# Kernel tuning notes

Hardware: AMD Instinct MI355X
Metric: run time of the kernel (lower is better)

## Reference

```python
import jax, jax.numpy as jnp
import numpy as np

N_QUBITS = 12
N_LAYERS = 4
SCALE = 1.0
BATCH = 256


def setup_inputs() -> dict:
    key = jax.random.key(0)
    k1, k2, k3 = jax.random.split(key, 3)
    return {
        "x": jax.random.normal(k1, (BATCH, N_QUBITS), dtype=jnp.float32),
        "weights": jax.random.normal(k2, (N_LAYERS, N_QUBITS, 3), dtype=jnp.float32),
        "entanglers": jax.random.uniform(k3, (N_LAYERS, N_QUBITS), dtype=jnp.float32),
    }


def _ry(theta):
    # theta: () or (B,) -> (..., 2, 2) complex64.  RY = [[c,-s],[s,c]]
    c = jnp.cos(theta / 2)
    s = jnp.sin(theta / 2)
    return jnp.stack([jnp.stack([c, -s], -1), jnp.stack([s, c], -1)], -2).astype(jnp.complex64)


def _rz(theta):
    # RZ = diag(e^{-i t/2}, e^{+i t/2})
    e = jnp.exp(-1j * theta.astype(jnp.complex64) / 2)
    z = jnp.zeros_like(e)
    return jnp.stack([jnp.stack([e, z], -1), jnp.stack([z, jnp.conj(e)], -1)], -2)


def _apply_1q(psi, U, q, n):
    # psi: (B, 2**n), wire 0 = most significant bit (PennyLane convention)
    B = psi.shape[0]
    psi = psi.reshape(B, 2 ** q, 2, 2 ** (n - q - 1))
    if U.ndim == 2:  # shared gate (weights)
        psi = jnp.einsum("ij,bajc->baic", U, psi)
    else:  # per-sample gate (inputs)
        psi = jnp.einsum("bij,bajc->baic", U, psi)
    return psi.reshape(B, 2 ** n)


def _apply_cnot(psi, c, t, n):
    # control c, target t (distinct), handles wrap-around since moveaxis is general
    B = psi.shape[0]
    psi = psi.reshape((B,) + (2,) * n)
    psi = jnp.moveaxis(psi, (c + 1, t + 1), (1, 2))
    shp = psi.shape
    psi = psi.reshape(B, 2, 2, -1)
    psi = jnp.stack([psi[:, 0], psi[:, 1, ::-1]], axis=1)  # flip target where control=1
    psi = psi.reshape(shp)
    psi = jnp.moveaxis(psi, (1, 2), (c + 1, t + 1))
    return psi.reshape(B, 2 ** n)


def reference(x, weights, entanglers):
    n = N_QUBITS
    B = x.shape[0]
    pi = jnp.float32(np.pi)
    psi = jnp.zeros((B, 2 ** n), jnp.complex64).at[:, 0].set(1.0)
    # encoding: RY(x_i * pi) then RZ(x_i^2 * pi) per qubit (per-sample gates)
    for q in range(n):
        psi = _apply_1q(psi, _ry(x[:, q] * pi), q, n)
        psi = _apply_1q(psi, _rz((x[:, q] ** 2) * pi), q, n)
    mask = entanglers > 0.5
    for layer in range(N_LAYERS):
        for q in range(n):
            phi, th, om = weights[layer, q, 0], weights[layer, q, 1], weights[layer, q, 2]
            U = _rz(om) @ _ry(th) @ _rz(phi)  # PennyLane Rot(phi, theta, omega)
            psi = _apply_1q(psi, U, q, n)
        for q in range(n):
            psi2 = _apply_cnot(psi, q, (q + 1) % n, n)
            psi = jnp.where(mask[layer, q], psi2, psi)
    probs = psi.real ** 2 + psi.imag ** 2  # (B, 2**n)
    # <Z_q> = sum_s p(s) * (1 - 2*bit_q(s)); wire 0 is MSB
    bits = (jnp.arange(2 ** n)[:, None] >> jnp.arange(n - 1, -1, -1)[None, :]) & 1
    signs = (1 - 2 * bits).astype(jnp.float32)  # (2**n, n)
    return (probs @ signs) * jnp.float32(SCALE)
```

## Files before the change

kernel.cpp:

```cpp
#include <hip/hip_runtime.h>
#include <math.h>

constexpr int NQ  = 12;
constexpr int NS  = 1 << NQ;
constexpr int NL  = 4;
constexpr int BLK = 256;
constexpr int R   = 16;
constexpr float PI_F = 3.14159265358979323846f;


typedef float c32 __attribute__((ext_vector_type(2)));

__device__ __forceinline__ c32 cmul(c32 a, c32 b) {
    c32 t = (c32){-a.y, a.y} * b.yx;
    return (c32){a.x, a.x} * b + t;
}
struct cg { c32 xx, ny; };
__device__ __forceinline__ cg mkg(c32 u) {
    cg g; g.xx = (c32){u.x, u.x}; g.ny = (c32){-u.y, u.y}; return g;
}
__device__ __forceinline__ c32 cmulg(cg g, c32 b) { return g.xx * b + g.ny * b.yx; }
__device__ __forceinline__ c32 cmadg(cg g, c32 b, c32 c) { return g.xx * b + (g.ny * b.yx + c); }

__device__ __forceinline__ void sfence() { __builtin_amdgcn_sched_barrier(0); }

template<int CTRL>
__device__ __forceinline__ float dppmov(float v) {
    return __int_as_float(__builtin_amdgcn_mov_dpp(__float_as_int(v), CTRL, 0xF, 0xF, false));
}
__device__ __forceinline__ float dppx4(float v) {
    int s = __float_as_int(v);
    int o = __builtin_amdgcn_update_dpp(s, s, 0x104, 0xF, 0x5, false);
    o     = __builtin_amdgcn_update_dpp(o, s, 0x114, 0xF, 0xA, false);
    return __int_as_float(o);
}

#if __has_builtin(__builtin_amdgcn_permlane16_swap)
#define HAVE_PL16 1
#endif
#if __has_builtin(__builtin_amdgcn_permlane32_swap)
#define HAVE_PL32 1
#endif

template<int M>
__device__ __forceinline__ float lanex(float v, int tid) {
    if constexpr (M == 1)  return dppmov<0xB1>(v);
    else if constexpr (M == 2)  return dppmov<0x4E>(v);
    else if constexpr (M == 4)  return dppx4(v);
    else if constexpr (M == 8)  return dppmov<0x128>(v);
    else if constexpr (M == 16) {
#ifdef HAVE_PL16
        auto r = __builtin_amdgcn_permlane16_swap(__float_as_int(v), __float_as_int(v), false, false);
        return __int_as_float((tid & 16) ? r[0] : r[1]);
#else
        return __shfl_xor(v, 16, 64);
#endif
    } else {
#ifdef HAVE_PL32
        auto r = __builtin_amdgcn_permlane32_swap(__float_as_int(v), __float_as_int(v), false, false);
        return __int_as_float((tid & 32) ? r[0] : r[1]);
#else
        return __shfl_xor(v, 32, 64);
#endif
    }
}
template<int M>
__device__ __forceinline__ c32 cx(c32 v, int tid) {
    return (c32){lanex<M>(v.x, tid), lanex<M>(v.y, tid)};
}

template<int P>
__device__ __forceinline__ void gate_reg(c32* v, const c32* u) {
    const cg g00 = mkg(u[0]), g01 = mkg(u[1]), g10 = mkg(u[2]), g11 = mkg(u[3]);
    #pragma unroll
    for (int r = 0; r < R; ++r)
        if (!(r & (1 << P))) {
            c32 a = v[r], b = v[r | (1 << P)];
            v[r]            = cmadg(g01, b, cmulg(g00, a));
            v[r | (1 << P)] = cmadg(g11, b, cmulg(g10, a));
        }
}

template<int M>
__device__ __forceinline__ void gate_lane(c32* v, int tid, const c32* u) {
    const bool hi = tid & M;
    const c32 Ud = hi ? u[3] : u[0];
    const c32 Uo = hi ? u[2] : u[1];
    const cg gd = mkg(Ud), go = mkg(Uo);
    c32 o[R];
    #pragma unroll
    for (int r = 0; r < R; ++r) o[r] = cx<M>(v[r], tid);
    sfence();
    #pragma unroll
    for (int r = 0; r < R; ++r) v[r] = cmadg(gd, v[r], cmulg(go, o[r]));
}

template<int CM, int TM>
__device__ __forceinline__ void cnot_ll(c32* v, int tid) {
    if (tid & CM) {
        c32 o[R];
        #pragma unroll
        for (int r = 0; r < R; ++r) o[r] = cx<TM>(v[r], tid);
        sfence();
        #pragma unroll
        for (int r = 0; r < R; ++r) v[r] = o[r];
    }
}

template<int PC, int PT>
__device__ __forceinline__ void cnot_rr(c32* v) {
    #pragma unroll
    for (int r = 0; r < R; ++r)
        if ((r & (1 << PC)) && !(r & (1 << PT))) {
            c32 t = v[r]; v[r] = v[r ^ (1 << PT)]; v[r ^ (1 << PT)] = t;
        }
}

__global__ __launch_bounds__(BLK, 1)
void qsim_kernel(const float* __restrict__ x,
                 const float* __restrict__ w,
                 const float* __restrict__ ent,
                 float* __restrict__ out)
{
    __shared__ c32  xbuf[NS];
    __shared__ c32  gmat[NL * NQ][4];
    __shared__ c32  uenc[NQ][2];
    __shared__ int  entf[NL * NQ];
    __shared__ float redbuf[4 * NQ];

    const int tid = threadIdx.x;
    const int b   = blockIdx.x;

    if (tid < NL * NQ) {
        float phi = w[tid * 3 + 0], th = w[tid * 3 + 1], om = w[tid * 3 + 2];
        float s, c;   sincosf(0.5f * th, &s, &c);
        float sa, ca; sincosf(0.5f * (phi + om), &sa, &ca);
        float sm, cm; sincosf(0.5f * (phi - om), &sm, &cm);
        gmat[tid][0] = (c32){ c * ca, -c * sa};
        gmat[tid][1] = (c32){-s * cm, -s * sm};
        gmat[tid][2] = (c32){ s * cm, -s * sm};
        gmat[tid][3] = (c32){ c * ca,  c * sa};
        entf[tid] = ent[tid] > 0.5f;
    }
    if (tid >= 64 && tid < 64 + NQ) {
        int q = tid - 64;
        float xv = x[b * NQ + q];
        float s, c;   sincosf(0.5f * PI_F * xv, &s, &c);
        float zs, zc; sincosf(0.5f * PI_F * xv * xv, &zs, &zc);
        uenc[q][0] = (c32){c * zc, -c * zs};
        uenc[q][1] = (c32){s * zc,  s * zs};
    }
    __syncthreads();

    c32 A = uenc[0][(tid >> 7) & 1];
    #pragma unroll
    for (int q = 1; q < 8; ++q) A = cmul(A, uenc[q][(tid >> (7 - q)) & 1]);
    c32 AP[4], PAB[4];
    #pragma unroll
    for (int j = 0; j < 4; ++j)
        AP[j] = cmul(A, cmul(uenc[8][j >> 1], uenc[9][j & 1]));
    #pragma unroll
    for (int k = 0; k < 4; ++k)
        PAB[k] = cmul(uenc[10][k >> 1], uenc[11][k & 1]);
    c32 v[R];
    #pragma unroll
    for (int r = 0; r < R; ++r) v[r] = cmul(AP[(r >> 2) & 3], PAB[r & 3]);

    const int lane_slot = tid & 63;
    const int g         = tid >> 6;

    #pragma unroll 1
    for (int layer = 0; layer < NL; ++layer) {
        const int gb = layer * NQ;

        {
            #pragma unroll
            for (int r = 0; r < R; ++r) xbuf[r * BLK + tid] = v[r];

            const c32* Ua = gmat[gb + 0];
            const c32* Ub = gmat[gb + 1];
            const int  gp = (entf[gb + 0] && (g & 2)) ? (g ^ 1) : g;
            const int  ar = (gp >> 1) * 2, br = (gp & 1) * 2;
            c32 K0 = cmul(Ua[ar + ( g      >> 1)], Ub[br + ( g      & 1)]);
            c32 K1 = cmul(Ua[ar + ((g ^ 1) >> 1)], Ub[br + ((g ^ 1) & 1)]);
            c32 K2 = cmul(Ua[ar + ((g ^ 2) >> 1)], Ub[br + ((g ^ 2) & 1)]);
            c32 K3 = cmul(Ua[ar + ((g ^ 3) >> 1)], Ub[br + ((g ^ 3) & 1)]);
            const bool pf = (layer > 0) && entf[gb - 1];
            const cg gE0 = mkg(K0), gE1 = mkg(K1), gE2 = mkg(K2), gE3 = mkg(K3);
            const cg gO0 = mkg(pf ? K2 : K0), gO1 = mkg(pf ? K3 : K1);
            const cg gO2 = mkg(pf ? K0 : K2), gO3 = mkg(pf ? K1 : K3);

            const c32* p1 = xbuf + ((g ^ 1) << 6) + lane_slot;
            const c32* p2 = xbuf + ((g ^ 2) << 6) + lane_slot;
            const c32* p3 = xbuf + ((g ^ 3) << 6) + lane_slot;

            __syncthreads();
            c32 b1[R], b2[R], b3[R];
            #pragma unroll
            for (int r = 0; r < R; ++r) b1[r] = p1[r * BLK];
            #pragma unroll
            for (int r = 0; r < R; ++r) b2[r] = p2[r * BLK];
            #pragma unroll
            for (int r = 0; r < R; ++r) b3[r] = p3[r * BLK];
            sfence();
            #pragma unroll
            for (int r = 0; r < R; ++r) {
                c32 acc;
                if (r & 1) {
                    acc = cmulg(gO0, v[r]);
                    acc = cmadg(gO1, b1[r], acc);
                    acc = cmadg(gO2, b2[r], acc);
                    acc = cmadg(gO3, b3[r], acc);
                } else {
                    acc = cmulg(gE0, v[r]);
                    acc = cmadg(gE1, b1[r], acc);
                    acc = cmadg(gE2, b2[r], acc);
                    acc = cmadg(gE3, b3[r], acc);
                }
                v[r] = acc;
            }
            __syncthreads();
        }

        gate_lane<32>(v, tid, gmat[gb + 2]);
        gate_lane<16>(v, tid, gmat[gb + 3]);
        gate_lane< 8>(v, tid, gmat[gb + 4]);
        gate_lane< 4>(v, tid, gmat[gb + 5]);
        gate_lane< 2>(v, tid, gmat[gb + 6]);
        gate_lane< 1>(v, tid, gmat[gb + 7]);
        gate_reg<3>(v, gmat[gb + 8]);
        gate_reg<2>(v, gmat[gb + 9]);
        gate_reg<1>(v, gmat[gb + 10]);
        gate_reg<0>(v, gmat[gb + 11]);

        if (entf[gb + 1] && (tid & 64)) {
            c32 o[R];
            #pragma unroll
            for (int r = 0; r < R; ++r) o[r] = cx<32>(v[r], tid);
            sfence();
            #pragma unroll
            for (int r = 0; r < R; ++r) v[r] = o[r];
        }
        if (entf[gb + 2]) cnot_ll<32, 16>(v, tid);
        if (entf[gb + 3]) cnot_ll<16,  8>(v, tid);
        if (entf[gb + 4]) cnot_ll< 8,  4>(v, tid);
        if (entf[gb + 5]) cnot_ll< 4,  2>(v, tid);
        if (entf[gb + 6]) cnot_ll< 2,  1>(v, tid);
        if (entf[gb + 7]) {
            const bool c_ = tid & 1;
            #pragma unroll
            for (int r = 0; r < 8; ++r) {
                c32 a = v[r], bb = v[r | 8];
                v[r]     = c_ ? bb : a;
                v[r | 8] = c_ ? a  : bb;
            }
        }
        if (entf[gb + 8])  cnot_rr<3, 2>(v);
        if (entf[gb + 9])  cnot_rr<2, 1>(v);
        if (entf[gb + 10]) cnot_rr<1, 0>(v);
    }

    const bool e011L = entf[(NL - 1) * NQ + 11];
    const int  t7    = (tid >> 7) & 1;

    float pr[R];
    #pragma unroll
    for (int r = 0; r < R; ++r) {
        c32 p = v[r] * v[r];
        pr[r] = p.x + p.y;
    }
    float S = 0.f, acc0 = 0.f;
    #pragma unroll
    for (int r = 0; r < R; ++r) {
        S += pr[r];
        const int s11 = t7 ^ (e011L & (r & 1));
        acc0 += s11 ? -pr[r] : pr[r];
    }
    float T[4];
    #pragma unroll
    for (int pb = 0; pb < 4; ++pb) {
        float t = 0.f;
        #pragma unroll
        for (int r = 0; r < R; ++r) t += ((r >> pb) & 1) ? -pr[r] : pr[r];
        T[pb] = t;
    }

    float contrib[NQ];
    contrib[0] = acc0;
    #pragma unroll
    for (int q = 1; q < 8; ++q) contrib[q] = ((tid >> (7 - q)) & 1) ? -S : S;
    contrib[8] = T[3]; contrib[9] = T[2]; contrib[10] = T[1]; contrib[11] = T[0];

    #pragma unroll
    for (int step = 0; step < 6; ++step) {
        float o[NQ];
        #pragma unroll
        for (int q = 0; q < NQ; ++q) {
            switch (step) {
                case 0: o[q] = lanex< 1>(contrib[q], tid); break;
                case 1: o[q] = lanex< 2>(contrib[q], tid); break;
                case 2: o[q] = lanex< 4>(contrib[q], tid); break;
                case 3: o[q] = lanex< 8>(contrib[q], tid); break;
                case 4: o[q] = lanex<16>(contrib[q], tid); break;
                default: o[q] = lanex<32>(contrib[q], tid); break;
            }
        }
        #pragma unroll
        for (int q = 0; q < NQ; ++q) contrib[q] += o[q];
    }
    if ((tid & 63) == 0) {
        const int wv = tid >> 6;
        #pragma unroll
        for (int q = 0; q < NQ; ++q) redbuf[wv * NQ + q] = contrib[q];
    }
    __syncthreads();
    if (tid < NQ)
        out[b * NQ + tid] = redbuf[tid] + redbuf[NQ + tid] + redbuf[2 * NQ + tid] + redbuf[3 * NQ + tid];
}

extern "C" void kernel_launch(void* const* d_in, const int* in_sizes, int n_in,
                              void* d_out, int out_size, void* d_ws, size_t ws_size,
                              hipStream_t stream) {
    const float* x   = (const float*)d_in[0];
    const float* w   = (const float*)d_in[1];
    const float* ent = (const float*)d_in[2];
    float* out = (float*)d_out;
    const int B = in_sizes[0] / NQ;
    qsim_kernel<<<B, BLK, 0, stream>>>(x, w, ent, out);
}
```

Before: 78.44 us.

## Double threads per block, halve registers per thread, fuse three qubits in LDS stage

Raises the block to 512 threads with 8 amplitudes per thread instead of 16, so qubits 0-2 are spread across wave groups. The LDS exchange stage now applies a fused three-qubit gate (an 8x8 Kronecker product with the CNOT permutations folded in) through shared memory, replacing the earlier two-qubit version. The aim is more waves per CU and fewer registers per thread to hide latency. The cost is 8-term complex accumulations per amplitude and more LDS reads per element, and the reduction now spans 8 waves.

```diff
diff --git a/kernel.cpp b/kernel.cpp
--- a/kernel.cpp
+++ b/kernel.cpp
@@ -4,8 +4,8 @@
 constexpr int NQ  = 12;
 constexpr int NS  = 1 << NQ;
 constexpr int NL  = 4;
-constexpr int BLK = 256;
-constexpr int R   = 16;
+constexpr int BLK = 512;
+constexpr int R   = 8;
 constexpr float PI_F = 3.14159265358979323846f;
 
 
@@ -116,7 +116,7 @@
         }
 }
 
-__global__ __launch_bounds__(BLK, 1)
+__global__ __launch_bounds__(BLK, 2)
 void qsim_kernel(const float* __restrict__ x,
                  const float* __restrict__ w,
                  const float* __restrict__ ent,
@@ -126,7 +126,7 @@
     __shared__ c32  gmat[NL * NQ][4];
     __shared__ c32  uenc[NQ][2];
     __shared__ int  entf[NL * NQ];
-    __shared__ float redbuf[4 * NQ];
+    __shared__ float redbuf[8 * NQ];
 
     const int tid = threadIdx.x;
     const int b   = blockIdx.x;
@@ -152,19 +152,16 @@
     }
     __syncthreads();
 
-    c32 A = uenc[0][(tid >> 7) & 1];
-    #pragma unroll
-    for (int q = 1; q < 8; ++q) A = cmul(A, uenc[q][(tid >> (7 - q)) & 1]);
-    c32 AP[4], PAB[4];
-    #pragma unroll
-    for (int j = 0; j < 4; ++j)
-        AP[j] = cmul(A, cmul(uenc[8][j >> 1], uenc[9][j & 1]));
-    #pragma unroll
-    for (int k = 0; k < 4; ++k)
-        PAB[k] = cmul(uenc[10][k >> 1], uenc[11][k & 1]);
+    c32 A = uenc[0][(tid >> 8) & 1];
+    #pragma unroll
+    for (int q = 1; q < 9; ++q) A = cmul(A, uenc[q][(tid >> (8 - q)) & 1]);
+    c32 PB[R];
+    #pragma unroll
+    for (int k = 0; k < R; ++k)
+        PB[k] = cmul(uenc[9][(k >> 2) & 1], cmul(uenc[10][(k >> 1) & 1], uenc[11][k & 1]));
     c32 v[R];
     #pragma unroll
-    for (int r = 0; r < R; ++r) v[r] = cmul(AP[(r >> 2) & 3], PAB[r & 3]);
+    for (int r = 0; r < R; ++r) v[r] = cmul(A, PB[r]);
 
     const int lane_slot = tid & 63;
     const int g         = tid >> 6;
@@ -179,61 +176,126 @@
 
             const c32* Ua = gmat[gb + 0];
             const c32* Ub = gmat[gb + 1];
-            const int  gp = (entf[gb + 0] && (g & 2)) ? (g ^ 1) : g;
-            const int  ar = (gp >> 1) * 2, br = (gp & 1) * 2;
-            c32 K0 = cmul(Ua[ar + ( g      >> 1)], Ub[br + ( g      & 1)]);
-            c32 K1 = cmul(Ua[ar + ((g ^ 1) >> 1)], Ub[br + ((g ^ 1) & 1)]);
-            c32 K2 = cmul(Ua[ar + ((g ^ 2) >> 1)], Ub[br + ((g ^ 2) & 1)]);
-            c32 K3 = cmul(Ua[ar + ((g ^ 3) >> 1)], Ub[br + ((g ^ 3) & 1)]);
+            const c32* Uc = gmat[gb + 2];
+            int gp = (entf[gb + 1] && (g & 2)) ? (g ^ 1) : g;
+            gp     = (entf[gb + 0] && (gp & 4)) ? (gp ^ 2) : gp;
+            const int ar = (gp >> 2) * 2;
+            const int br = ((gp >> 1) & 1) * 2;
+            const int cr = (gp & 1) * 2;
+            cg gE[8];
+            #pragma unroll
+            for (int m = 0; m < 8; ++m) {
+                const int j = g ^ m;
+                c32 kk = cmul(Ua[ar + (j >> 2)],
+                          cmul(Ub[br + ((j >> 1) & 1)], Uc[cr + (j & 1)]));
+                gE[m] = mkg(kk);
+            }
             const bool pf = (layer > 0) && entf[gb - 1];
-            const cg gE0 = mkg(K0), gE1 = mkg(K1), gE2 = mkg(K2), gE3 = mkg(K3);
-            const cg gO0 = mkg(pf ? K2 : K0), gO1 = mkg(pf ? K3 : K1);
-            const cg gO2 = mkg(pf ? K0 : K2), gO3 = mkg(pf ? K1 : K3);
-
-            const c32* p1 = xbuf + ((g ^ 1) << 6) + lane_slot;
-            const c32* p2 = xbuf + ((g ^ 2) << 6) + lane_slot;
-            const c32* p3 = xbuf + ((g ^ 3) << 6) + lane_slot;
+
+            const c32* px = xbuf + lane_slot;
 
             __syncthreads();
-            c32 b1[R], b2[R], b3[R];
-            #pragma unroll
-            for (int r = 0; r < R; ++r) b1[r] = p1[r * BLK];
-            #pragma unroll
-            for (int r = 0; r < R; ++r) b2[r] = p2[r * BLK];
-            #pragma unroll
-            for (int r = 0; r < R; ++r) b3[r] = p3[r * BLK];
-            sfence();
-            #pragma unroll
-            for (int r = 0; r < R; ++r) {
-                c32 acc;
-                if (r & 1) {
-                    acc = cmulg(gO0, v[r]);
-                    acc = cmadg(gO1, b1[r], acc);
-                    acc = cmadg(gO2, b2[r], acc);
-                    acc = cmadg(gO3, b3[r], acc);
-                } else {
-                    acc = cmulg(gE0, v[r]);
-                    acc = cmadg(gE1, b1[r], acc);
-                    acc = cmadg(gE2, b2[r], acc);
-                    acc = cmadg(gE3, b3[r], acc);
+            {
+                c32 bm[7][4];
+                #pragma unroll
+                for (int m = 1; m < 8; ++m) {
+                    const c32* pp = px + ((g ^ m) << 6);
+                    #pragma unroll
+                    for (int r = 0; r < 4; ++r) bm[m - 1][r] = pp[r * BLK];
                 }
-                v[r] = acc;
+                sfence();
+                #pragma unroll
+                for (int r = 0; r < 4; ++r) {
+                    c32 acc;
+                    if (!(r & 1)) {
+                        acc = cmulg(gE[0], v[r]);
+                        acc = cmadg(gE[1], bm[0][r], acc);
+                        acc = cmadg(gE[2], bm[1][r], acc);
+                        acc = cmadg(gE[3], bm[2][r], acc);
+                        acc = cmadg(gE[4], bm[3][r], acc);
+                        acc = cmadg(gE[5], bm[4][r], acc);
+                        acc = cmadg(gE[6], bm[5][r], acc);
+                        acc = cmadg(gE[7], bm[6][r], acc);
+                    } else if (!pf) {
+                        acc = cmulg(gE[0], v[r]);
+                        acc = cmadg(gE[1], bm[0][r], acc);
+                        acc = cmadg(gE[2], bm[1][r], acc);
+                        acc = cmadg(gE[3], bm[2][r], acc);
+                        acc = cmadg(gE[4], bm[3][r], acc);
+                        acc = cmadg(gE[5], bm[4][r], acc);
+                        acc = cmadg(gE[6], bm[5][r], acc);
+                        acc = cmadg(gE[7], bm[6][r], acc);
+                    } else {
+                        acc = cmulg(gE[4], v[r]);
+                        acc = cmadg(gE[5], bm[0][r], acc);
+                        acc = cmadg(gE[6], bm[1][r], acc);
+                        acc = cmadg(gE[7], bm[2][r], acc);
+                        acc = cmadg(gE[0], bm[3][r], acc);
+                        acc = cmadg(gE[1], bm[4][r], acc);
+                        acc = cmadg(gE[2], bm[5][r], acc);
+                        acc = cmadg(gE[3], bm[6][r], acc);
+                    }
+                    v[r] = acc;
+                }
+            }
+            {
+                c32 bm[7][4];
+                #pragma unroll
+                for (int m = 1; m < 8; ++m) {
+                    const c32* pp = px + ((g ^ m) << 6) + 4 * BLK;
+                    #pragma unroll
+                    for (int r = 0; r < 4; ++r) bm[m - 1][r] = pp[r * BLK];
+                }
+                sfence();
+                #pragma unroll
+                for (int rr = 0; rr < 4; ++rr) {
+                    const int r = rr + 4;
+                    c32 acc;
+                    if (!(r & 1)) {
+                        acc = cmulg(gE[0], v[r]);
+                        acc = cmadg(gE[1], bm[0][rr], acc);
+                        acc = cmadg(gE[2], bm[1][rr], acc);
+                        acc = cmadg(gE[3], bm[2][rr], acc);
+                        acc = cmadg(gE[4], bm[3][rr], acc);
+                        acc = cmadg(gE[5], bm[4][rr], acc);
+                        acc = cmadg(gE[6], bm[5][rr], acc);
+                        acc = cmadg(gE[7], bm[6][rr], acc);
+                    } else if (!pf) {
+                        acc = cmulg(gE[0], v[r]);
+                        acc = cmadg(gE[1], bm[0][rr], acc);
+                        acc = cmadg(gE[2], bm[1][rr], acc);
+                        acc = cmadg(gE[3], bm[2][rr], acc);
+                        acc = cmadg(gE[4], bm[3][rr], acc);
+                        acc = cmadg(gE[5], bm[4][rr], acc);
+                        acc = cmadg(gE[6], bm[5][rr], acc);
+                        acc = cmadg(gE[7], bm[6][rr], acc);
+                    } else {
+                        acc = cmulg(gE[4], v[r]);
+                        acc = cmadg(gE[5], bm[0][rr], acc);
+                        acc = cmadg(gE[6], bm[1][rr], acc);
+                        acc = cmadg(gE[7], bm[2][rr], acc);
+                        acc = cmadg(gE[0], bm[3][rr], acc);
+                        acc = cmadg(gE[1], bm[4][rr], acc);
+                        acc = cmadg(gE[2], bm[5][rr], acc);
+                        acc = cmadg(gE[3], bm[6][rr], acc);
+                    }
+                    v[r] = acc;
+                }
             }
             __syncthreads();
         }
 
-        gate_lane<32>(v, tid, gmat[gb + 2]);
-        gate_lane<16>(v, tid, gmat[gb + 3]);
-        gate_lane< 8>(v, tid, gmat[gb + 4]);
-        gate_lane< 4>(v, tid, gmat[gb + 5]);
-        gate_lane< 2>(v, tid, gmat[gb + 6]);
-        gate_lane< 1>(v, tid, gmat[gb + 7]);
-        gate_reg<3>(v, gmat[gb + 8]);
+        gate_lane<32>(v, tid, gmat[gb + 3]);
+        gate_lane<16>(v, tid, gmat[gb + 4]);
+        gate_lane< 8>(v, tid, gmat[gb + 5]);
+        gate_lane< 4>(v, tid, gmat[gb + 6]);
+        gate_lane< 2>(v, tid, gmat[gb + 7]);
+        gate_lane< 1>(v, tid, gmat[gb + 8]);
         gate_reg<2>(v, gmat[gb + 9]);
         gate_reg<1>(v, gmat[gb + 10]);
         gate_reg<0>(v, gmat[gb + 11]);
 
-        if (entf[gb + 1] && (tid & 64)) {
+        if (entf[gb + 2] && (tid & 64)) {
             c32 o[R];
             #pragma unroll
             for (int r = 0; r < R; ++r) o[r] = cx<32>(v[r], tid);
@@ -241,27 +303,26 @@
             #pragma unroll
             for (int r = 0; r < R; ++r) v[r] = o[r];
         }
-        if (entf[gb + 2]) cnot_ll<32, 16>(v, tid);
-        if (entf[gb + 3]) cnot_ll<16,  8>(v, tid);
-        if (entf[gb + 4]) cnot_ll< 8,  4>(v, tid);
-        if (entf[gb + 5]) cnot_ll< 4,  2>(v, tid);
-        if (entf[gb + 6]) cnot_ll< 2,  1>(v, tid);
-        if (entf[gb + 7]) {
+        if (entf[gb + 3]) cnot_ll<32, 16>(v, tid);
+        if (entf[gb + 4]) cnot_ll<16,  8>(v, tid);
+        if (entf[gb + 5]) cnot_ll< 8,  4>(v, tid);
+        if (entf[gb + 6]) cnot_ll< 4,  2>(v, tid);
+        if (entf[gb + 7]) cnot_ll< 2,  1>(v, tid);
+        if (entf[gb + 8]) {
             const bool c_ = tid & 1;
             #pragma unroll
-            for (int r = 0; r < 8; ++r) {
-                c32 a = v[r], bb = v[r | 8];
+            for (int r = 0; r < 4; ++r) {
+                c32 a = v[r], bb = v[r | 4];
                 v[r]     = c_ ? bb : a;
-                v[r | 8] = c_ ? a  : bb;
-            }
-        }
-        if (entf[gb + 8])  cnot_rr<3, 2>(v);
+                v[r | 4] = c_ ? a  : bb;
+            }
+        }
         if (entf[gb + 9])  cnot_rr<2, 1>(v);
         if (entf[gb + 10]) cnot_rr<1, 0>(v);
     }
 
     const bool e011L = entf[(NL - 1) * NQ + 11];
-    const int  t7    = (tid >> 7) & 1;
+    const int  t8    = (tid >> 8) & 1;
 
     float pr[R];
     #pragma unroll
@@ -273,12 +334,12 @@
     #pragma unroll
     for (int r = 0; r < R; ++r) {
         S += pr[r];
-        const int s11 = t7 ^ (e011L & (r & 1));
+        const int s11 = t8 ^ (e011L & (r & 1));
         acc0 += s11 ? -pr[r] : pr[r];
     }
-    float T[4];
-    #pragma unroll
-    for (int pb = 0; pb < 4; ++pb) {
+    float T[3];
+    #pragma unroll
+    for (int pb = 0; pb < 3; ++pb) {
         float t = 0.f;
         #pragma unroll
         for (int r = 0; r < R; ++r) t += ((r >> pb) & 1) ? -pr[r] : pr[r];
@@ -288,8 +349,8 @@
     float contrib[NQ];
     contrib[0] = acc0;
     #pragma unroll
-    for (int q = 1; q < 8; ++q) contrib[q] = ((tid >> (7 - q)) & 1) ? -S : S;
-    contrib[8] = T[3]; contrib[9] = T[2]; contrib[10] = T[1]; contrib[11] = T[0];
+    for (int q = 1; q < 9; ++q) contrib[q] = ((tid >> (8 - q)) & 1) ? -S : S;
+    contrib[9] = T[2]; contrib[10] = T[1]; contrib[11] = T[0];
 
     #pragma unroll
     for (int step = 0; step < 6; ++step) {
@@ -314,8 +375,12 @@
         for (int q = 0; q < NQ; ++q) redbuf[wv * NQ + q] = contrib[q];
     }
     __syncthreads();
-    if (tid < NQ)
-        out[b * NQ + tid] = redbuf[tid] + redbuf[NQ + tid] + redbuf[2 * NQ + tid] + redbuf[3 * NQ + tid];
+    if (tid < NQ) {
+        float s = 0.f;
+        #pragma unroll
+        for (int wv = 0; wv < 8; ++wv) s += redbuf[wv * NQ + tid];
+        out[b * NQ + tid] = s;
+    }
 }
 
 extern "C" void kernel_launch(void* const* d_in, const int* in_sizes, int n_in,
```

Measured after the change: 80.30 us. +2.4%, slower.
